# Optimization experiments

Measured on AMD Instinct MI355X. Metric: run time of the kernel, lower is better.

The kernel has to match this reference:

```python
import jax, jax.numpy as jnp
import numpy as np

NUM_EMBEDDINGS = 8192
EMBEDDING_DIM = 512
COMMITMENT_COST = 0.25
N_INPUTS = 32768


def setup_inputs() -> dict:
    key = jax.random.key(0)
    k1, k2 = jax.random.split(key)
    inputs = jax.random.normal(k1, (N_INPUTS, EMBEDDING_DIM), dtype=jnp.float32)
    weight = jax.random.normal(k2, (NUM_EMBEDDINGS, EMBEDDING_DIM), dtype=jnp.float32)
    return {"inputs": inputs, "weight": weight}


def reference(inputs, weight):
    # distances[n, k] = ||x_n||^2 + ||w_k||^2 - 2 x_n . w_k   -> [N, K]
    distances = (
        jnp.sum(inputs ** 2, axis=1, keepdims=True)
        + jnp.sum(weight ** 2, axis=1)
        - 2.0 * (inputs @ weight.T)
    )
    probs = jax.nn.softmax(-distances, axis=-1)            # [N, K]
    idx = jnp.argmin(distances, axis=1)                    # [N]
    quantized = weight[idx]                                # gather == one-hot @ weight

    e_latent_loss = jnp.mean((jax.lax.stop_gradient(quantized) - inputs) ** 2)
    q_latent_loss = jnp.mean((quantized - jax.lax.stop_gradient(inputs)) ** 2)
    loss = q_latent_loss + COMMITMENT_COST * e_latent_loss

    # straight-through estimator
    quantized_st = inputs + jax.lax.stop_gradient(quantized - inputs)

    # avg over one-hot encodings == normalized code histogram
    counts = jnp.bincount(idx, length=NUM_EMBEDDINGS).astype(inputs.dtype)
    avg_probs = counts / inputs.shape[0]
    perplexity = jnp.exp(-jnp.sum(avg_probs * jnp.log(avg_probs + 1e-10)))

    return (quantized_st, probs, loss, perplexity)
```

## Files before the change

### kernel.cpp

```cpp
#include <hip/hip_runtime.h>
#include <hip/hip_fp16.h>
#include <math.h>

#define N_ROWS 32768
#define K_CODES 8192
#define DIM 512

#define OUT_Q 0
#define OUT_P ((size_t)N_ROWS * DIM)
#define OUT_LOSS (OUT_P + (size_t)N_ROWS * K_CODES)
#define OUT_PERP (OUT_LOSS + 1)

#define WS_WSQ 0
#define WS_CNT (K_CODES)
#define WS_ERR (2 * K_CODES)
#define WS_RED (2 * K_CODES + N_ROWS)
#define WS_F16 (2 * K_CODES + N_ROWS + 64)

#define XH_OFF ((size_t)0)
#define XL_OFF ((size_t)N_ROWS * DIM)
#define WH_OFF ((size_t)2 * N_ROWS * DIM)
#define WL_OFF ((size_t)2 * N_ROWS * DIM + (size_t)K_CODES * DIM)
#define F16_COUNT ((size_t)2 * (N_ROWS + K_CODES) * DIM)
#define WS_NEEDED ((size_t)WS_F16 * 4 + F16_COUNT * 2)

typedef _Float16 f16x8 __attribute__((ext_vector_type(8)));
typedef float f32x4 __attribute__((ext_vector_type(4)));

__device__ inline void load_lds16(const void* g, void* l) {
    __builtin_amdgcn_global_load_lds((const __attribute__((address_space(1))) void*)g,
                                     (__attribute__((address_space(3))) void*)l,
                                     16, 0, 0);
}

__device__ inline unsigned int fkey(float f) {
    unsigned int b = __float_as_uint(f);
    return b ^ ((unsigned int)((int)b >> 31) | 0x80000000u);
}
__device__ inline float fkey_inv(unsigned int k) {
    unsigned int b = (k & 0x80000000u) ? (k ^ 0x80000000u) : ~k;
    return __uint_as_float(b);
}

__global__ void wsq_kernel(const float* __restrict__ W, float* __restrict__ ws) {
    int row = blockIdx.x;
    int lane = threadIdx.x;
    const float* src = W + (size_t)row * DIM;
    float4 v0 = *(const float4*)(src + lane * 8);
    float4 v1 = *(const float4*)(src + lane * 8 + 4);
    float s = v0.x * v0.x + v0.y * v0.y + v0.z * v0.z + v0.w * v0.w
            + v1.x * v1.x + v1.y * v1.y + v1.z * v1.z + v1.w * v1.w;
#pragma unroll
    for (int off = 32; off > 0; off >>= 1) s += __shfl_down(s, off, 64);
    if (lane == 0) ws[WS_WSQ + row] = s;
}

__global__ void __launch_bounds__(256) convert_split_kernel(
    const float* __restrict__ X, const float* __restrict__ W,
    _Float16* __restrict__ f16base, float* __restrict__ ws) {
    const size_t NX8 = (size_t)N_ROWS * DIM / 8;
    size_t t = (size_t)blockIdx.x * 256 + threadIdx.x;
    const float* src;
    _Float16 *hd, *ld;
    bool isW = (t >= NX8);
    if (!isW) {
        src = X + t * 8;
        hd = f16base + XH_OFF + t * 8;
        ld = f16base + XL_OFF + t * 8;
    } else {
        size_t u = t - NX8;
        src = W + u * 8;
        hd = f16base + WH_OFF + u * 8;
        ld = f16base + WL_OFF + u * 8;
    }
    float4 v0 = *(const float4*)src;
    float4 v1 = *(const float4*)(src + 4);
    float v[8] = {v0.x, v0.y, v0.z, v0.w, v1.x, v1.y, v1.z, v1.w};
    f16x8 h, l;
    float s = 0.f;
#pragma unroll
    for (int i = 0; i < 8; ++i) {
        _Float16 hv = (_Float16)v[i];
        h[i] = hv;
        l[i] = (_Float16)(v[i] - (float)hv);
        s += v[i] * v[i];
    }
    *(f16x8*)hd = h;
    *(f16x8*)ld = l;
    if (isW) {
#pragma unroll
        for (int off = 32; off > 0; off >>= 1) s += __shfl_down(s, off, 64);
        if ((threadIdx.x & 63) == 0) ws[WS_WSQ + ((t - NX8) >> 6)] = s;
    }
}

#define LDSB 24576
#define AH_O 0
#define AL_O 8192
#define BH_O 16384
#define BL_O 20480

__global__ void __launch_bounds__(512, 2) gemm_dist_mfma_kernel(
    const _Float16* __restrict__ f16base, const float* __restrict__ ws,
    float* __restrict__ out) {
    __shared__ _Float16 lds[3 * LDSB];

    const int tid = threadIdx.x;
    const int w = tid >> 6;
    const int lane = tid & 63;

    int lin = blockIdx.y * 64 + blockIdx.x;
    int xcd = lin & 7;
    int idx = lin >> 3;
    const int bn = (xcd * 8 + (idx & 7)) * 128;
    const int bm = (idx >> 3) * 256;

    const int wr = w >> 1;
    const int wc = w & 1;
    const int q = lane >> 4;
    const int fm = lane & 15;
    const int l4 = lane >> 2;
    const int p = lane & 3;

    f32x4 acc[4][4];
#pragma unroll
    for (int i = 0; i < 4; ++i)
#pragma unroll
        for (int j = 0; j < 4; ++j) acc[i][j] = (f32x4){0.f, 0.f, 0.f, 0.f};

    auto stage = [&](int ks, _Float16* buf, int part) {
        const int kk = ks * 32;
        int g = w * 2 + part;
        int arow = g * 16 + l4;
        int ca = p ^ ((arow >> 1) & 3);
        size_t aoff = (size_t)(bm + arow) * DIM + kk + ca * 8;
        load_lds16(f16base + XH_OFF + aoff, buf + AH_O + g * 512);
        load_lds16(f16base + XL_OFF + aoff, buf + AL_O + g * 512);
        int brow = w * 16 + l4;
        int cb = p ^ ((brow >> 1) & 3);
        size_t boff = (size_t)(bn + brow) * DIM + kk + cb * 8;
        if (part == 0)
            load_lds16(f16base + WH_OFF + boff, buf + BH_O + w * 512);
        else
            load_lds16(f16base + WL_OFF + boff, buf + BL_O + w * 512);
    };

    _Float16* c0 = lds;
    _Float16* c1 = lds + LDSB;
    _Float16* c2 = lds + 2 * LDSB;

    stage(0, c0, 0); stage(0, c0, 1);
    stage(1, c1, 0); stage(1, c1, 1);
    asm volatile("s_waitcnt vmcnt(6)" ::: "memory");
    __builtin_amdgcn_s_barrier();
    __builtin_amdgcn_sched_barrier(0);

#pragma unroll 1
    for (int ks = 0; ks < 16; ++ks) {
        if (ks < 14) { stage(ks + 2, c2, 0); stage(ks + 2, c2, 1); }

        f16x8 bhv[4], blv[4], ahv[4], alv[4];
#pragma unroll
        for (int j = 0; j < 4; ++j) {
            int bb = wc * 64 + j * 16 + fm;
            int off = bb * 32 + ((q ^ ((bb >> 1) & 3)) * 8);
            bhv[j] = *(const f16x8*)&c0[BH_O + off];
            blv[j] = *(const f16x8*)&c0[BL_O + off];
        }
#pragma unroll
        for (int i = 0; i < 4; ++i) {
            int am = wr * 64 + i * 16 + fm;
            int off = am * 32 + ((q ^ ((am >> 1) & 3)) * 8);
            ahv[i] = *(const f16x8*)&c0[AH_O + off];
            alv[i] = *(const f16x8*)&c0[AL_O + off];
        }

        __builtin_amdgcn_s_setprio(1);
#pragma unroll
        for (int i = 0; i < 4; ++i)
#pragma unroll
            for (int j = 0; j < 4; ++j) {
                acc[i][j] = __builtin_amdgcn_mfma_f32_16x16x32_f16(
                    ahv[i], bhv[j], acc[i][j], 0, 0, 0);
                acc[i][j] = __builtin_amdgcn_mfma_f32_16x16x32_f16(
                    ahv[i], blv[j], acc[i][j], 0, 0, 0);
                acc[i][j] = __builtin_amdgcn_mfma_f32_16x16x32_f16(
                    alv[i], bhv[j], acc[i][j], 0, 0, 0);
            }
        __builtin_amdgcn_s_setprio(0);

        if (ks < 14) {
            asm volatile("s_waitcnt vmcnt(6)" ::: "memory");
        } else if (ks == 14) {
            asm volatile("s_waitcnt vmcnt(0)" ::: "memory");
        }
        __builtin_amdgcn_s_barrier();
        __builtin_amdgcn_sched_barrier(0);

        _Float16* t0 = c0; c0 = c1; c1 = c2; c2 = t0;
    }

    const float* wsq = ws + WS_WSQ;
    float* Dout = out + OUT_P;
    const int q4 = q * 4;
#pragma unroll
    for (int i = 0; i < 4; ++i) {
#pragma unroll
        for (int j = 0; j < 4; ++j) {
            int n = bn + wc * 64 + j * 16 + fm;
            float wn = wsq[n];
#pragma unroll
            for (int r = 0; r < 4; ++r) {
                int m = bm + wr * 64 + i * 16 + q4 + r;
                Dout[(size_t)m * K_CODES + n] = wn - 2.f * acc[i][j][r];
            }
        }
    }
}

#define BM 128
#define BN 128
#define BK 16

__global__ void __launch_bounds__(256) gemm_dist_fp32_kernel(
    const float* __restrict__ X, const float* __restrict__ W,
    const float* __restrict__ ws, float* __restrict__ out) {
    __shared__ float As[BK][BM];
    __shared__ float Bs[BK][BN];

    const int bn = blockIdx.x * BN;
    const int bm = blockIdx.y * BM;
    const int tid = threadIdx.x;
    const int tx = tid & 15;
    const int ty = tid >> 4;
    const int lr = tid >> 1;
    const int lc = (tid & 1) * 8;

    float acc[8][8];
#pragma unroll
    for (int i = 0; i < 8; ++i)
#pragma unroll
        for (int j = 0; j < 8; ++j) acc[i][j] = 0.f;

    const float* aptr = X + (size_t)(bm + lr) * DIM + lc;
    const float* bptr = W + (size_t)(bn + lr) * DIM + lc;

    for (int k0 = 0; k0 < DIM; k0 += BK) {
        float4 a0 = *(const float4*)(aptr + k0);
        float4 a1 = *(const float4*)(aptr + k0 + 4);
        float4 b0 = *(const float4*)(bptr + k0);
        float4 b1 = *(const float4*)(bptr + k0 + 4);
        __syncthreads();
        As[lc + 0][lr] = a0.x; As[lc + 1][lr] = a0.y;
        As[lc + 2][lr] = a0.z; As[lc + 3][lr] = a0.w;
        As[lc + 4][lr] = a1.x; As[lc + 5][lr] = a1.y;
        As[lc + 6][lr] = a1.z; As[lc + 7][lr] = a1.w;
        Bs[lc + 0][lr] = b0.x; Bs[lc + 1][lr] = b0.y;
        Bs[lc + 2][lr] = b0.z; Bs[lc + 3][lr] = b0.w;
        Bs[lc + 4][lr] = b1.x; Bs[lc + 5][lr] = b1.y;
        Bs[lc + 6][lr] = b1.z; Bs[lc + 7][lr] = b1.w;
        __syncthreads();
#pragma unroll
        for (int kk = 0; kk < BK; ++kk) {
            float a[8], b[8];
            *(float4*)&a[0] = *(const float4*)&As[kk][ty * 8];
            *(float4*)&a[4] = *(const float4*)&As[kk][ty * 8 + 4];
            *(float4*)&b[0] = *(const float4*)&Bs[kk][tx * 8];
            *(float4*)&b[4] = *(const float4*)&Bs[kk][tx * 8 + 4];
#pragma unroll
            for (int i = 0; i < 8; ++i)
#pragma unroll
                for (int j = 0; j < 8; ++j)
                    acc[i][j] = fmaf(a[i], b[j], acc[i][j]);
        }
    }

    const float* wsq = ws + WS_WSQ;
    const int m0 = bm + ty * 8;
    const int n0 = bn + tx * 8;
    float wn[8];
    *(float4*)&wn[0] = *(const float4*)(wsq + n0);
    *(float4*)&wn[4] = *(const float4*)(wsq + n0 + 4);
    float* Dout = out + OUT_P;
#pragma unroll
    for (int i = 0; i < 8; ++i) {
        float4 o0, o1;
        o0.x = wn[0] - 2.f * acc[i][0];
        o0.y = wn[1] - 2.f * acc[i][1];
        o0.z = wn[2] - 2.f * acc[i][2];
        o0.w = wn[3] - 2.f * acc[i][3];
        o1.x = wn[4] - 2.f * acc[i][4];
        o1.y = wn[5] - 2.f * acc[i][5];
        o1.z = wn[6] - 2.f * acc[i][6];
        o1.w = wn[7] - 2.f * acc[i][7];
        float* drow = Dout + (size_t)(m0 + i) * K_CODES + n0;
        *(float4*)(drow) = o0;
        *(float4*)(drow + 4) = o1;
    }
}

__global__ void __launch_bounds__(512) probs_quant_kernel(
    const float* __restrict__ X, const float* __restrict__ W,
    float* __restrict__ out, float* __restrict__ ws) {
    const int n = blockIdx.x;
    const int tid = threadIdx.x;
    __shared__ unsigned long long mred[8];
    __shared__ float fred[8];

    float4* Drow4 = (float4*)(out + OUT_P + (size_t)n * K_CODES);

    const float x = X[(size_t)n * DIM + tid];

    float4 e[4];
    unsigned long long best = ~0ull;
#pragma unroll
    for (int t = 0; t < 4; ++t) {
        float4 v = Drow4[tid + t * 512];
        e[t] = v;
        unsigned int c0 = (unsigned int)((tid + t * 512) * 4);
        unsigned long long k;
        k = ((unsigned long long)fkey(v.x) << 32) | (c0 + 0u);
        best = k < best ? k : best;
        k = ((unsigned long long)fkey(v.y) << 32) | (c0 + 1u);
        best = k < best ? k : best;
        k = ((unsigned long long)fkey(v.z) << 32) | (c0 + 2u);
        best = k < best ? k : best;
        k = ((unsigned long long)fkey(v.w) << 32) | (c0 + 3u);
        best = k < best ? k : best;
    }
#pragma unroll
    for (int d = 1; d < 64; d <<= 1) {
        unsigned long long o = __shfl_xor(best, d, 64);
        best = o < best ? o : best;
    }
    if ((tid & 63) == 0) mred[tid >> 6] = best;
    __syncthreads();
    unsigned long long bm = mred[0];
#pragma unroll
    for (int i = 1; i < 8; ++i) bm = mred[i] < bm ? mred[i] : bm;
    const float smin = fkey_inv((unsigned int)(bm >> 32));
    const int amin = (int)(bm & 0xFFFFFFFFu);

    float sum = 0.f;
#pragma unroll
    for (int t = 0; t < 4; ++t) {
        float4 v = e[t];
        float4 ev;
        ev.x = __expf(smin - v.x);
        ev.y = __expf(smin - v.y);
        ev.z = __expf(smin - v.z);
        ev.w = __expf(smin - v.w);
        e[t] = ev;
        sum += ev.x + ev.y + ev.z + ev.w;
    }
#pragma unroll
    for (int off = 32; off > 0; off >>= 1) sum += __shfl_down(sum, off, 64);
    if ((tid & 63) == 0) fred[tid >> 6] = sum;
    __syncthreads();
    float tot = fred[0];
#pragma unroll
    for (int i = 1; i < 8; ++i) tot += fred[i];
    const float inv = 1.0f / tot;

#pragma unroll
    for (int t = 0; t < 4; ++t) {
        float4 ev = e[t];
        ev.x *= inv; ev.y *= inv; ev.z *= inv; ev.w *= inv;
        Drow4[tid + t * 512] = ev;
    }

    const float qv = W[(size_t)amin * DIM + tid];
    out[OUT_Q + (size_t)n * DIM + tid] = qv;
    float d2 = qv - x;
    float err = d2 * d2;
#pragma unroll
    for (int off = 32; off > 0; off >>= 1) err += __shfl_down(err, off, 64);
    __syncthreads();
    if ((tid & 63) == 0) fred[tid >> 6] = err;
    __syncthreads();
    if (tid == 0) {
        float e8 = fred[0];
#pragma unroll
        for (int i = 1; i < 8; ++i) e8 += fred[i];
        ws[WS_ERR + n] = e8;
        atomicAdd(ws + WS_CNT + amin, 1.0f);
    }
}

__global__ void __launch_bounds__(256) finalize_part_kernel(
    float* __restrict__ ws) {
    __shared__ float red[256];
    const int b = blockIdx.x;
    const int tid = threadIdx.x;

    float errsum = 0.f;
    const int ebase = b * 1024;
#pragma unroll
    for (int j = tid; j < 1024; j += 256) errsum += ws[WS_ERR + ebase + j];

    float p = ws[WS_CNT + b * 256 + tid] * (1.0f / (float)N_ROWS);
    float ent = -p * logf(p + 1e-10f);

    red[tid] = errsum;
    __syncthreads();
    for (int st = 128; st > 0; st >>= 1) {
        if (tid < st) red[tid] += red[tid + st];
        __syncthreads();
    }
    if (tid == 0) ws[WS_RED + b] = red[0];
    __syncthreads();
    red[tid] = ent;
    __syncthreads();
    for (int st = 128; st > 0; st >>= 1) {
        if (tid < st) red[tid] += red[tid + st];
        __syncthreads();
    }
    if (tid == 0) ws[WS_RED + 32 + b] = red[0];
}

__global__ void __launch_bounds__(64) finalize_fin_kernel(
    float* __restrict__ out, const float* __restrict__ ws) {
    const int tid = threadIdx.x;
    float ev = tid < 32 ? ws[WS_RED + tid] : 0.f;
    float nv = tid < 32 ? ws[WS_RED + 32 + tid] : 0.f;
#pragma unroll
    for (int off = 32; off > 0; off >>= 1) {
        ev += __shfl_down(ev, off, 64);
        nv += __shfl_down(nv, off, 64);
    }
    if (tid == 0) {
        float mse = ev * (1.0f / ((float)N_ROWS * (float)DIM));
        out[OUT_LOSS] = mse + 0.25f * mse;
        out[OUT_PERP] = expf(nv);
    }
}

extern "C" void kernel_launch(void* const* d_in, const int* in_sizes, int n_in,
                              void* d_out, int out_size, void* d_ws, size_t ws_size,
                              hipStream_t stream) {
    const float* X = (const float*)d_in[0];
    const float* W = (const float*)d_in[1];
    float* out = (float*)d_out;
    float* ws = (float*)d_ws;

    hipMemsetAsync(ws + WS_CNT, 0, K_CODES * sizeof(float), stream);

    if (ws_size >= WS_NEEDED) {
        _Float16* f16base = (_Float16*)(ws + WS_F16);
        const int conv_blocks =
            (int)(((size_t)(N_ROWS + K_CODES) * DIM / 8 + 255) / 256);
        convert_split_kernel<<<conv_blocks, 256, 0, stream>>>(X, W, f16base, ws);

        dim3 ggrid(64, 128);
        gemm_dist_mfma_kernel<<<ggrid, 512, 0, stream>>>(f16base, ws, out);
    } else {
        wsq_kernel<<<K_CODES, 64, 0, stream>>>(W, ws);
        dim3 ggrid(K_CODES / BN, N_ROWS / BM);
        gemm_dist_fp32_kernel<<<ggrid, 256, 0, stream>>>(X, W, ws, out);
    }

    probs_quant_kernel<<<N_ROWS, 512, 0, stream>>>(X, W, out, ws);
    finalize_part_kernel<<<32, 256, 0, stream>>>(ws);
    finalize_fin_kernel<<<1, 64, 0, stream>>>(out, ws);
}
```

Before: 2.349 ms.

## Use nontemporal memory ops, split GEMM k-step into halves, process two rows per softmax block

Converted fp16 operands and the distance matrix writes now use nontemporal stores, and the softmax kernel reads and writes with nontemporal loads and stores to reduce cache pollution on the large probs stream. The MFMA loop is split into two half-tiles, each with its own staging call and an extra barrier, so global-to-LDS prefetch is interleaved with compute and fewer A registers are live. The probs kernel now uses 256 threads handling two rows per block, and the second row's loads are issued before the first row's exp pass so memory latency overlaps compute. These changes add register pressure, add a barrier per k-step, and rely on nontemporal hints behaving well for data that is re-read soon after.

After: 2.261 ms. -3.7%, faster.

```diff
diff --git a/kernel.cpp b/kernel.cpp
--- a/kernel.cpp
+++ b/kernel.cpp
@@ -15,7 +15,7 @@
 #define WS_CNT (K_CODES)
 #define WS_ERR (2 * K_CODES)
 #define WS_RED (2 * K_CODES + N_ROWS)
-#define WS_F16 (2 * K_CODES + N_ROWS + 64)
+#define WS_F16 (WS_RED + 64)
 
 #define XH_OFF ((size_t)0)
 #define XL_OFF ((size_t)N_ROWS * DIM)
@@ -26,11 +26,23 @@
 
 typedef _Float16 f16x8 __attribute__((ext_vector_type(8)));
 typedef float f32x4 __attribute__((ext_vector_type(4)));
+typedef float f32x2 __attribute__((ext_vector_type(2)));
+typedef unsigned long long u64;
 
 __device__ inline void load_lds16(const void* g, void* l) {
     __builtin_amdgcn_global_load_lds((const __attribute__((address_space(1))) void*)g,
                                      (__attribute__((address_space(3))) void*)l,
                                      16, 0, 0);
+}
+
+__device__ inline f32x4 ntload4(const float* p) {
+    return __builtin_nontemporal_load((const f32x4*)p);
+}
+__device__ inline void ntstore4(float* p, f32x4 v) {
+    __builtin_nontemporal_store(v, (f32x4*)p);
+}
+__device__ inline void ntstore1(float* p, float v) {
+    __builtin_nontemporal_store(v, p);
 }
 
 __device__ inline unsigned int fkey(float f) {
@@ -85,8 +97,8 @@
         l[i] = (_Float16)(v[i] - (float)hv);
         s += v[i] * v[i];
     }
-    *(f16x8*)hd = h;
-    *(f16x8*)ld = l;
+    __builtin_nontemporal_store(h, (f16x8*)hd);
+    __builtin_nontemporal_store(l, (f16x8*)ld);
     if (isW) {
 #pragma unroll
         for (int off = 32; off > 0; off >>= 1) s += __shfl_down(s, off, 64);
@@ -103,7 +115,7 @@
 __global__ void __launch_bounds__(512, 2) gemm_dist_mfma_kernel(
     const _Float16* __restrict__ f16base, const float* __restrict__ ws,
     float* __restrict__ out) {
-    __shared__ _Float16 lds[3 * LDSB];
+    __shared__ __align__(16) _Float16 lds[3 * LDSB];
 
     const int tid = threadIdx.x;
     const int w = tid >> 6;
@@ -157,9 +169,7 @@
 
 #pragma unroll 1
     for (int ks = 0; ks < 16; ++ks) {
-        if (ks < 14) { stage(ks + 2, c2, 0); stage(ks + 2, c2, 1); }
-
-        f16x8 bhv[4], blv[4], ahv[4], alv[4];
+        f16x8 bhv[4], blv[4];
 #pragma unroll
         for (int j = 0; j < 4; ++j) {
             int bb = wc * 64 + j * 16 + fm;
@@ -167,28 +177,51 @@
             bhv[j] = *(const f16x8*)&c0[BH_O + off];
             blv[j] = *(const f16x8*)&c0[BL_O + off];
         }
-#pragma unroll
-        for (int i = 0; i < 4; ++i) {
+        f16x8 ah[2], al[2];
+#pragma unroll
+        for (int i = 0; i < 2; ++i) {
             int am = wr * 64 + i * 16 + fm;
             int off = am * 32 + ((q ^ ((am >> 1) & 3)) * 8);
-            ahv[i] = *(const f16x8*)&c0[AH_O + off];
-            alv[i] = *(const f16x8*)&c0[AL_O + off];
-        }
-
+            ah[i] = *(const f16x8*)&c0[AH_O + off];
+            al[i] = *(const f16x8*)&c0[AL_O + off];
+        }
+        if (ks < 14) stage(ks + 2, c2, 0);
         __builtin_amdgcn_s_setprio(1);
 #pragma unroll
-        for (int i = 0; i < 4; ++i)
+        for (int i = 0; i < 2; ++i)
 #pragma unroll
             for (int j = 0; j < 4; ++j) {
                 acc[i][j] = __builtin_amdgcn_mfma_f32_16x16x32_f16(
-                    ahv[i], bhv[j], acc[i][j], 0, 0, 0);
+                    ah[i], bhv[j], acc[i][j], 0, 0, 0);
                 acc[i][j] = __builtin_amdgcn_mfma_f32_16x16x32_f16(
-                    ahv[i], blv[j], acc[i][j], 0, 0, 0);
+                    ah[i], blv[j], acc[i][j], 0, 0, 0);
                 acc[i][j] = __builtin_amdgcn_mfma_f32_16x16x32_f16(
-                    alv[i], bhv[j], acc[i][j], 0, 0, 0);
+                    al[i], bhv[j], acc[i][j], 0, 0, 0);
             }
         __builtin_amdgcn_s_setprio(0);
-
+        __builtin_amdgcn_s_barrier();
+
+#pragma unroll
+        for (int i = 0; i < 2; ++i) {
+            int am = wr * 64 + (i + 2) * 16 + fm;
+            int off = am * 32 + ((q ^ ((am >> 1) & 3)) * 8);
+            ah[i] = *(const f16x8*)&c0[AH_O + off];
+            al[i] = *(const f16x8*)&c0[AL_O + off];
+        }
+        if (ks < 14) stage(ks + 2, c2, 1);
+        __builtin_amdgcn_s_setprio(1);
+#pragma unroll
+        for (int i = 0; i < 2; ++i)
+#pragma unroll
+            for (int j = 0; j < 4; ++j) {
+                acc[i + 2][j] = __builtin_amdgcn_mfma_f32_16x16x32_f16(
+                    ah[i], bhv[j], acc[i + 2][j], 0, 0, 0);
+                acc[i + 2][j] = __builtin_amdgcn_mfma_f32_16x16x32_f16(
+                    ah[i], blv[j], acc[i + 2][j], 0, 0, 0);
+                acc[i + 2][j] = __builtin_amdgcn_mfma_f32_16x16x32_f16(
+                    al[i], bhv[j], acc[i + 2][j], 0, 0, 0);
+            }
+        __builtin_amdgcn_s_setprio(0);
         if (ks < 14) {
             asm volatile("s_waitcnt vmcnt(6)" ::: "memory");
         } else if (ks == 14) {
@@ -212,7 +245,8 @@
 #pragma unroll
             for (int r = 0; r < 4; ++r) {
                 int m = bm + wr * 64 + i * 16 + q4 + r;
-                Dout[(size_t)m * K_CODES + n] = wn - 2.f * acc[i][j][r];
+                ntstore1(&Dout[(size_t)m * K_CODES + n],
+                         wn - 2.f * acc[i][j][r]);
             }
         }
     }
@@ -299,91 +333,155 @@
     }
 }
 
-__global__ void __launch_bounds__(512) probs_quant_kernel(
+__global__ void __launch_bounds__(256) probs_quant_kernel(
     const float* __restrict__ X, const float* __restrict__ W,
     float* __restrict__ out, float* __restrict__ ws) {
-    const int n = blockIdx.x;
     const int tid = threadIdx.x;
-    __shared__ unsigned long long mred[8];
-    __shared__ float fred[8];
-
-    float4* Drow4 = (float4*)(out + OUT_P + (size_t)n * K_CODES);
-
-    const float x = X[(size_t)n * DIM + tid];
-
-    float4 e[4];
-    unsigned long long best = ~0ull;
-#pragma unroll
-    for (int t = 0; t < 4; ++t) {
-        float4 v = Drow4[tid + t * 512];
-        e[t] = v;
-        unsigned int c0 = (unsigned int)((tid + t * 512) * 4);
-        unsigned long long k;
-        k = ((unsigned long long)fkey(v.x) << 32) | (c0 + 0u);
-        best = k < best ? k : best;
-        k = ((unsigned long long)fkey(v.y) << 32) | (c0 + 1u);
-        best = k < best ? k : best;
-        k = ((unsigned long long)fkey(v.z) << 32) | (c0 + 2u);
-        best = k < best ? k : best;
-        k = ((unsigned long long)fkey(v.w) << 32) | (c0 + 3u);
-        best = k < best ? k : best;
+    const int wv = tid >> 6;
+    const int rA = blockIdx.x;
+    const int rB = blockIdx.x + N_ROWS / 2;
+    __shared__ u64 mred[4];
+    __shared__ float sred[4];
+    __shared__ float ered[4];
+
+    float* DA = out + OUT_P + (size_t)rA * K_CODES;
+    float* DB = out + OUT_P + (size_t)rB * K_CODES;
+
+    f32x2 xA = ((const f32x2*)(X + (size_t)rA * DIM))[tid];
+    f32x2 xB = ((const f32x2*)(X + (size_t)rB * DIM))[tid];
+
+    f32x4 eA[8];
+#pragma unroll
+    for (int t = 0; t < 8; ++t) eA[t] = ntload4(DA + (tid + t * 256) * 4);
+
+    u64 bestA = ~0ull;
+#pragma unroll
+    for (int t = 0; t < 8; ++t) {
+        unsigned int c0 = (unsigned int)((tid + t * 256) * 4);
+#pragma unroll
+        for (int c = 0; c < 4; ++c) {
+            u64 k = ((u64)fkey(eA[t][c]) << 32) | (c0 + c);
+            bestA = k < bestA ? k : bestA;
+        }
     }
 #pragma unroll
     for (int d = 1; d < 64; d <<= 1) {
-        unsigned long long o = __shfl_xor(best, d, 64);
-        best = o < best ? o : best;
-    }
-    if ((tid & 63) == 0) mred[tid >> 6] = best;
-    __syncthreads();
-    unsigned long long bm = mred[0];
-#pragma unroll
-    for (int i = 1; i < 8; ++i) bm = mred[i] < bm ? mred[i] : bm;
-    const float smin = fkey_inv((unsigned int)(bm >> 32));
-    const int amin = (int)(bm & 0xFFFFFFFFu);
-
-    float sum = 0.f;
-#pragma unroll
-    for (int t = 0; t < 4; ++t) {
-        float4 v = e[t];
-        float4 ev;
-        ev.x = __expf(smin - v.x);
-        ev.y = __expf(smin - v.y);
-        ev.z = __expf(smin - v.z);
-        ev.w = __expf(smin - v.w);
-        e[t] = ev;
-        sum += ev.x + ev.y + ev.z + ev.w;
-    }
-#pragma unroll
-    for (int off = 32; off > 0; off >>= 1) sum += __shfl_down(sum, off, 64);
-    if ((tid & 63) == 0) fred[tid >> 6] = sum;
-    __syncthreads();
-    float tot = fred[0];
-#pragma unroll
-    for (int i = 1; i < 8; ++i) tot += fred[i];
-    const float inv = 1.0f / tot;
-
-#pragma unroll
-    for (int t = 0; t < 4; ++t) {
-        float4 ev = e[t];
-        ev.x *= inv; ev.y *= inv; ev.z *= inv; ev.w *= inv;
-        Drow4[tid + t * 512] = ev;
-    }
-
-    const float qv = W[(size_t)amin * DIM + tid];
-    out[OUT_Q + (size_t)n * DIM + tid] = qv;
-    float d2 = qv - x;
-    float err = d2 * d2;
-#pragma unroll
-    for (int off = 32; off > 0; off >>= 1) err += __shfl_down(err, off, 64);
-    __syncthreads();
-    if ((tid & 63) == 0) fred[tid >> 6] = err;
-    __syncthreads();
-    if (tid == 0) {
-        float e8 = fred[0];
-#pragma unroll
-        for (int i = 1; i < 8; ++i) e8 += fred[i];
-        ws[WS_ERR + n] = e8;
-        atomicAdd(ws + WS_CNT + amin, 1.0f);
+        u64 o = __shfl_xor(bestA, d, 64);
+        bestA = o < bestA ? o : bestA;
+    }
+    if ((tid & 63) == 0) mred[wv] = bestA;
+    __syncthreads();
+    u64 bmA = mred[0];
+#pragma unroll
+    for (int i = 1; i < 4; ++i) bmA = mred[i] < bmA ? mred[i] : bmA;
+    const float sminA = fkey_inv((unsigned int)(bmA >> 32));
+    const int aminA = (int)(bmA & 0xFFFFFFFFu);
+
+    f32x4 eB[8];
+#pragma unroll
+    for (int t = 0; t < 8; ++t) eB[t] = ntload4(DB + (tid + t * 256) * 4);
+
+    float sumA = 0.f;
+#pragma unroll
+    for (int t = 0; t < 8; ++t) {
+#pragma unroll
+        for (int c = 0; c < 4; ++c) {
+            float v = __expf(sminA - eA[t][c]);
+            eA[t][c] = v;
+            sumA += v;
+        }
+    }
+#pragma unroll
+    for (int off = 32; off > 0; off >>= 1) sumA += __shfl_down(sumA, off, 64);
+    if ((tid & 63) == 0) sred[wv] = sumA;
+    __syncthreads();
+    const float invA = 1.0f / (sred[0] + sred[1] + sred[2] + sred[3]);
+
+#pragma unroll
+    for (int t = 0; t < 8; ++t) {
+        f32x4 v = eA[t];
+        v *= invA;
+        ntstore4(DA + (tid + t * 256) * 4, v);
+    }
+
+    {
+        f32x2 wq = ((const f32x2*)(W + (size_t)aminA * DIM))[tid];
+        f32x2 d = wq - xA;
+        f32x2 o = xA + d;
+        __builtin_nontemporal_store(
+            o, (f32x2*)(out + OUT_Q + (size_t)rA * DIM) + tid);
+        float err = d.x * d.x + d.y * d.y;
+#pragma unroll
+        for (int off = 32; off > 0; off >>= 1) err += __shfl_down(err, off, 64);
+        if ((tid & 63) == 0) ered[wv] = err;
+        __syncthreads();
+        if (tid == 0) {
+            ws[WS_ERR + rA] = ered[0] + ered[1] + ered[2] + ered[3];
+            atomicAdd(ws + WS_CNT + aminA, 1.0f);
+        }
+    }
+
+    u64 bestB = ~0ull;
+#pragma unroll
+    for (int t = 0; t < 8; ++t) {
+        unsigned int c0 = (unsigned int)((tid + t * 256) * 4);
+#pragma unroll
+        for (int c = 0; c < 4; ++c) {
+            u64 k = ((u64)fkey(eB[t][c]) << 32) | (c0 + c);
+            bestB = k < bestB ? k : bestB;
+        }
+    }
+#pragma unroll
+    for (int d = 1; d < 64; d <<= 1) {
+        u64 o = __shfl_xor(bestB, d, 64);
+        bestB = o < bestB ? o : bestB;
+    }
+    if ((tid & 63) == 0) mred[wv] = bestB;
+    __syncthreads();
+    u64 bmB = mred[0];
+#pragma unroll
+    for (int i = 1; i < 4; ++i) bmB = mred[i] < bmB ? mred[i] : bmB;
+    const float sminB = fkey_inv((unsigned int)(bmB >> 32));
+    const int aminB = (int)(bmB & 0xFFFFFFFFu);
+
+    float sumB = 0.f;
+#pragma unroll
+    for (int t = 0; t < 8; ++t) {
+#pragma unroll
+        for (int c = 0; c < 4; ++c) {
+            float v = __expf(sminB - eB[t][c]);
+            eB[t][c] = v;
+            sumB += v;
+        }
+    }
+#pragma unroll
+    for (int off = 32; off > 0; off >>= 1) sumB += __shfl_down(sumB, off, 64);
+    if ((tid & 63) == 0) sred[wv] = sumB;
+    __syncthreads();
+    const float invB = 1.0f / (sred[0] + sred[1] + sred[2] + sred[3]);
+
+#pragma unroll
+    for (int t = 0; t < 8; ++t) {
+        f32x4 v = eB[t];
+        v *= invB;
+        ntstore4(DB + (tid + t * 256) * 4, v);
+    }
+
+    {
+        f32x2 wq = ((const f32x2*)(W + (size_t)aminB * DIM))[tid];
+        f32x2 d = wq - xB;
+        f32x2 o = xB + d;
+        __builtin_nontemporal_store(
+            o, (f32x2*)(out + OUT_Q + (size_t)rB * DIM) + tid);
+        float err = d.x * d.x + d.y * d.y;
+#pragma unroll
+        for (int off = 32; off > 0; off >>= 1) err += __shfl_down(err, off, 64);
+        if ((tid & 63) == 0) ered[wv] = err;
+        __syncthreads();
+        if (tid == 0) {
+            ws[WS_ERR + rB] = ered[0] + ered[1] + ered[2] + ered[3];
+            atomicAdd(ws + WS_CNT + aminB, 1.0f);
+        }
     }
 }
 
@@ -459,7 +557,7 @@
         gemm_dist_fp32_kernel<<<ggrid, 256, 0, stream>>>(X, W, ws, out);
     }
 
-    probs_quant_kernel<<<N_ROWS, 512, 0, stream>>>(X, W, out, ws);
+    probs_quant_kernel<<<N_ROWS / 2, 256, 0, stream>>>(X, W, out, ws);
     finalize_part_kernel<<<32, 256, 0, stream>>>(ws);
     finalize_fin_kernel<<<1, 64, 0, stream>>>(out, ws);
 }
```
